# Kernel tuning notes

Measured on AMD Instinct MI355X. Metric: run time of the kernel, lower is better.

Reference implementation:

```python
import jax, jax.numpy as jnp
import numpy as np
import math

B, T, O = 4, 1024, 128
D, H, L, V = 512, 8, 6, 128
M, EH = 100000, 4
EHD = D // EH
HD = D // H
TK = O + 2 * T
PAD_ID = 0
NGRAM = 4

def _primes():
    ps = []
    base = 131
    for h in range(EH):
        x = base + h * 1009
        row = []
        for _ in range(NGRAM):
            row.append(x % (2 ** 32))
            x = x * 31 + 1
        ps.append(row)
    return jnp.array(ps, dtype=jnp.uint32)

PRIMES = _primes()

def rmsnorm(x, scale, eps=1e-6):
    return x / jnp.sqrt(jnp.mean(jnp.square(x), axis=-1, keepdims=True) + eps) * scale

def precompute_freqs_cis(dim, max_len, theta=10000.0):
    freqs = 1.0 / theta ** (jnp.arange(0, dim, 2, dtype=jnp.float32) / dim)
    t = jnp.arange(max_len, dtype=jnp.float32)
    return jnp.exp(1j * jnp.outer(t, freqs))[None, :, None, :]  # (1, max_len, 1, dim/2)

def apply_rope(x, f):
    b, t, h, d = x.shape
    xc = jax.lax.complex(x[..., 0::2], x[..., 1::2])
    xr = xc * f
    return jnp.stack([xr.real, xr.imag], axis=-1).reshape(b, t, h, d)

def setup_inputs() -> dict:
    key = jax.random.key(0)
    ks = jax.random.split(key, 16)
    rn = lambda k, shp, s=0.02: jax.random.normal(k, shp, jnp.float32) * s
    logit = lambda p: float(np.log(p / (1.0 - p)))
    return {
        'tokens_w': jax.random.randint(ks[0], (B, T), 0, V, dtype=jnp.int32),
        'mem_ids': jax.random.randint(ks[1], (B, O), 0, V, dtype=jnp.int32),
        'mem_emb': jax.random.normal(ks[2], (B, O, D), jnp.float32),
        'ssum': jax.random.normal(ks[3], (B, D), jnp.float32),
        'embed_table': rn(ks[4], (V, D)),
        'engram_table': rn(ks[5], (M, EH, EHD)),
        'engram_gate': jnp.full((EH, EHD), -2.0, jnp.float32),
        'engram_scale': jnp.ones(D, jnp.float32),
        'mem_W': rn(ks[6], (D, D)), 'mem_b': jnp.zeros(D, jnp.float32),
        'mem_scale': jnp.ones(D, jnp.float32),
        'alpha_gate': jnp.full((D,), logit(0.1), jnp.float32),
        'ssum_W': rn(ks[7], (D, D)),
        'ln1': jnp.ones((L, D), jnp.float32),
        'qW': rn(ks[8], (L, D, D)), 'qb': jnp.zeros((L, D), jnp.float32),
        'kW': rn(ks[9], (L, D, D)), 'kb': jnp.zeros((L, D), jnp.float32),
        'vW': rn(ks[10], (L, D, D)), 'vb': jnp.zeros((L, D), jnp.float32),
        'oW': rn(ks[11], (L, D, D)), 'ob': jnp.zeros((L, D), jnp.float32),
        'ln2': jnp.ones((L, D), jnp.float32),
        'w_in': rn(ks[12], (L, D, 8 * D)),
        'w_out': rn(ks[13], (L, 4 * D, D)),
        'final_scale': jnp.ones(D, jnp.float32),
    }

def _forward(tokens_w, mem_ids, mem_emb, ssum, embed_table, engram_table, engram_gate,
             engram_scale, mem_W, mem_b, mem_scale, alpha_gate, ssum_W,
             ln1, qW, qb, kW, kb, vW, vb, oW, ob, ln2, w_in, w_out, final_scale):
    # token embedding
    x = embed_table[tokens_w]  # (B,T,D)
    # multi-head engram: rolling n-gram hash lookup
    cur = jnp.where(tokens_w == PAD_ID, 0, tokens_w).astype(jnp.uint32)
    prev = jnp.where(mem_ids == PAD_ID, 0, mem_ids).astype(jnp.uint32)
    full = jnp.concatenate([prev, cur], axis=1)  # (B, O+T)
    hs = jnp.zeros((B, T, EH), jnp.uint32)
    for i in range(NGRAM):
        chunk = full[:, O - i: O + T - i]
        hs = hs + chunk[:, :, None] * PRIMES[None, None, :, i]
    idx = (hs % jnp.uint32(M)).astype(jnp.int32)  # (B,T,EH)
    retr = engram_table[idx, jnp.arange(EH)[None, None, :], :]  # (B,T,EH,EHD)
    eng = (retr * jax.nn.sigmoid(engram_gate)[None, None]).reshape(B, T, D)
    eng = rmsnorm(eng, engram_scale)
    # memory adapter + state-sum injection
    mem_p = rmsnorm(mem_emb @ mem_W + mem_b, mem_scale)
    alpha = jax.nn.sigmoid(alpha_gate)
    x = x + (ssum @ ssum_W)[:, None, :] * alpha[None, None, :]
    kv_seq = jnp.concatenate([mem_p, eng, x], axis=1)  # (B, TK, D)
    # masks: mem fully visible, engram + current causal; pad invalid keys
    tril = jnp.tril(jnp.ones((T, T), bool))
    full_mask = jnp.concatenate([jnp.ones((T, O), bool), tril, tril], axis=1)
    valid_curr = tokens_w != PAD_ID
    valid_k = jnp.concatenate([jnp.ones((B, O), bool), valid_curr, valid_curr], axis=1)
    mask = full_mask[None, None] & valid_k[:, None, None, :]  # (B,1,T,TK)
    freqs = precompute_freqs_cis(HD, TK + 32)
    fq, fk = freqs[:, :T], freqs[:, :TK]
    scale = 1.0 / math.sqrt(HD)

    def block(cx, p):
        ln1_, qW_, qb_, kW_, kb_, vW_, vb_, oW_, ob_, ln2_, wi_, wo_ = p
        nx = rmsnorm(cx, ln1_)
        q = (nx @ qW_ + qb_).reshape(B, T, H, HD)
        k = (kv_seq @ kW_ + kb_).reshape(B, TK, H, HD)
        v = (kv_seq @ vW_ + vb_).reshape(B, TK, H, HD)
        q = apply_rope(q, fq)
        k = apply_rope(k, fk)
        scores = jnp.einsum('bqhd,bkhd->bhqk', q, k) * scale
        scores = jnp.where(mask, scores, -1e9)
        probs = jax.nn.softmax(scores, axis=-1)
        o = jnp.einsum('bhqk,bkhd->bqhd', probs, v).reshape(B, T, D)
        cx = cx + o @ oW_ + ob_
        n2 = rmsnorm(cx, ln2_)
        gate, val = jnp.split(n2 @ wi_, 2, axis=-1)
        cx = cx + (jax.nn.silu(gate) * val) @ wo_
        return cx, None

    curr_x, _ = jax.lax.scan(block, x, (ln1, qW, qb, kW, kb, vW, vb, oW, ob, ln2, w_in, w_out))
    return rmsnorm(curr_x, final_scale)

def reference(tokens_w, mem_ids, mem_emb, ssum, embed_table, engram_table, engram_gate,
              engram_scale, mem_W, mem_b, mem_scale, alpha_gate, ssum_W,
              ln1, qW, qb, kW, kb, vW, vb, oW, ob, ln2, w_in, w_out, final_scale):
    return _forward(tokens_w, mem_ids, mem_emb, ssum, embed_table, engram_table, engram_gate,
                    engram_scale, mem_W, mem_b, mem_scale, alpha_gate, ssum_W,
                    ln1, qW, qb, kW, kb, vW, vb, oW, ob, ln2, w_in, w_out, final_scale)
```

## Files before the change

kernel.cpp:

```cpp
#include <hip/hip_runtime.h>
#include <hip/hip_bf16.h>
#include <math.h>

#define B_ 4
#define T_ 1024
#define O_ 128
#define D_ 512
#define H_ 8
#define L_ 6
#define TK_ 2176
#define MM_ 100000
#define EH_ 4
#define EHD_ 128
#define HD_ 64

typedef float f32x4 __attribute__((ext_vector_type(4)));
typedef short bf16x8 __attribute__((ext_vector_type(8)));
typedef unsigned short u16;

__device__ __constant__ unsigned int PRIMES_[4][4] = {
  {131u,  4062u,  125923u, 3903614u},
  {1140u, 35341u, 1095572u, 33962733u},
  {2149u, 66620u, 2065221u, 64021852u},
  {3158u, 97899u, 3034870u, 94080971u},
};

__device__ __forceinline__ float wave_sum_f(float v) {
  #pragma unroll
  for (int off = 32; off; off >>= 1) v += __shfl_xor(v, off);
  return v;
}

__device__ __forceinline__ short f2bf(float f) {
  unsigned int u = __float_as_uint(f);
  unsigned int r = (u + 0x7fffu + ((u >> 16) & 1u)) >> 16;
  return (short)r;
}

__device__ __forceinline__ void gload16(const void* g, void* l) {
  __builtin_amdgcn_global_load_lds((const __attribute__((address_space(1))) void*)g,
                                   (__attribute__((address_space(3))) void*)l, 16, 0, 0);
}

__global__ __launch_bounds__(64) void rope_table_k(float* __restrict__ rc,
                                                   float* __restrict__ rs) {
  int i = blockIdx.x * 64 + threadIdx.x;
  int t = i >> 5, j = i & 31;
  float freq = __powf(10000.0f, -(float)j / 32.0f);
  float ang = (float)t * freq;
  rc[i] = cosf(ang);
  rs[i] = sinf(ang);
}

__global__ __launch_bounds__(256) void ssum_proj_k(const float* __restrict__ ssum,
                                                   const float* __restrict__ sW,
                                                   float* __restrict__ ssp) {
  int col = blockIdx.x * 256 + threadIdx.x;
  int b = blockIdx.y;
  float acc = 0.f;
  for (int d = 0; d < D_; ++d) acc += ssum[b * D_ + d] * sW[(size_t)d * D_ + col];
  ssp[b * D_ + col] = acc;
}

__global__ __launch_bounds__(256) void sgemm_k(const float* __restrict__ A,
                                               const float* __restrict__ W,
                                               const float* __restrict__ bias,
                                               float* __restrict__ C,
                                               int M, int N, int K) {
  __shared__ float As[16][68];
  __shared__ float Bs[16][68];
  int tid = threadIdx.x;
  int row0 = blockIdx.y * 64;
  int col0 = blockIdx.x * 64;
  int tx = tid & 15, ty = tid >> 4;
  int am = tid >> 2, ak = (tid & 3) * 4;
  int bk = tid >> 4, bc = (tid & 15) * 4;
  float acc[4][4] = {};
  for (int k0 = 0; k0 < K; k0 += 16) {
    float4 av = *reinterpret_cast<const float4*>(&A[(size_t)(row0 + am) * K + k0 + ak]);
    As[ak + 0][am] = av.x; As[ak + 1][am] = av.y; As[ak + 2][am] = av.z; As[ak + 3][am] = av.w;
    float4 bv = *reinterpret_cast<const float4*>(&W[(size_t)(k0 + bk) * N + col0 + bc]);
    *reinterpret_cast<float4*>(&Bs[bk][bc]) = bv;
    __syncthreads();
    #pragma unroll
    for (int kk = 0; kk < 16; ++kk) {
      float4 a4 = *reinterpret_cast<const float4*>(&As[kk][ty * 4]);
      float4 b4 = *reinterpret_cast<const float4*>(&Bs[kk][tx * 4]);
      float a[4] = {a4.x, a4.y, a4.z, a4.w};
      float b[4] = {b4.x, b4.y, b4.z, b4.w};
      #pragma unroll
      for (int i = 0; i < 4; ++i)
        #pragma unroll
        for (int j = 0; j < 4; ++j) acc[i][j] += a[i] * b[j];
    }
    __syncthreads();
  }
  int cbase = col0 + tx * 4;
  float4 b4 = *reinterpret_cast<const float4*>(&bias[cbase]);
  float bb[4] = {b4.x, b4.y, b4.z, b4.w};
  #pragma unroll
  for (int i = 0; i < 4; ++i) {
    int row = row0 + ty * 4 + i;
    *reinterpret_cast<float4*>(&C[(size_t)row * N + cbase]) =
        make_float4(acc[i][0] + bb[0], acc[i][1] + bb[1], acc[i][2] + bb[2], acc[i][3] + bb[3]);
  }
}

__device__ __forceinline__ void wconv_tile(const float* __restrict__ W, u16* __restrict__ wT,
                                           int K, int N) {
  __shared__ float s[64][65];
  int n0 = blockIdx.x * 64, k0 = blockIdx.y * 64;
  int tid = threadIdx.x;
  int kr = tid >> 4, nc = (tid & 15) * 4;
  #pragma unroll
  for (int kk = 0; kk < 4; ++kk) {
    float4 f = *reinterpret_cast<const float4*>(&W[(size_t)(k0 + kr + kk * 16) * N + n0 + nc]);
    s[kr + kk * 16][nc + 0] = f.x; s[kr + kk * 16][nc + 1] = f.y;
    s[kr + kk * 16][nc + 2] = f.z; s[kr + kk * 16][nc + 3] = f.w;
  }
  __syncthreads();
  int nr = tid >> 4, kc = (tid & 15) * 4;
  #pragma unroll
  for (int nn = 0; nn < 4; ++nn) {
    int n = nr + nn * 16;
    ushort4 o;
    o.x = (u16)f2bf(s[kc + 0][n]); o.y = (u16)f2bf(s[kc + 1][n]);
    o.z = (u16)f2bf(s[kc + 2][n]); o.w = (u16)f2bf(s[kc + 3][n]);
    *reinterpret_cast<ushort4*>(&wT[(size_t)(n0 + n) * K + k0 + kc]) = o;
  }
}

__global__ __launch_bounds__(256) void wconv_qkvo_k(const float* __restrict__ qW,
                                                    const float* __restrict__ kW,
                                                    const float* __restrict__ vW,
                                                    const float* __restrict__ oW,
                                                    u16* __restrict__ dst) {
  int z = blockIdx.z;
  int l = z >> 2, which = z & 3;
  const float* src = which == 0 ? qW : which == 1 ? kW : which == 2 ? vW : oW;
  wconv_tile(src + (size_t)l * D_ * D_, dst + (size_t)z * D_ * D_, D_, D_);
}

__global__ __launch_bounds__(256) void wconv_win_k(const float* __restrict__ w_in,
                                                   u16* __restrict__ dst) {
  int l = blockIdx.z;
  wconv_tile(w_in + (size_t)l * 512 * 4096, dst + (size_t)l * 4096 * 512, 512, 4096);
}

__global__ __launch_bounds__(256) void wconv_wout_k(const float* __restrict__ w_out,
                                                    u16* __restrict__ dst) {
  int l = blockIdx.z;
  wconv_tile(w_out + (size_t)l * 2048 * 512, dst + (size_t)l * 512 * 2048, 2048, 512);
}

template<int EPI>
__global__ __launch_bounds__(256) void gemm_sm_k(const u16* __restrict__ A,
                                                 const u16* __restrict__ Bt,
                                                 const float* __restrict__ bias,
                                                 void* __restrict__ Cout,
                                                 int M, int N, int K, int posmod,
                                                 const float* __restrict__ rc,
                                                 const float* __restrict__ rs) {
  __shared__ __align__(16) u16 As[2][64 * 32];
  __shared__ __align__(16) u16 Bs[2][64 * 32];
  int tid = threadIdx.x;
  int w = tid >> 6, lane = tid & 63;
  int lr = lane & 15, lg = lane >> 4;
  int row0 = blockIdx.y * 64, col0 = blockIdx.x * 64;
  int wr = w >> 1, wc = w & 1;
  f32x4 acc[2][2] = {};

  int srow = tid >> 2;
  int skel = (tid & 3) * 8;

  auto stage = [&](int buf, int k0) {
    gload16(A + (size_t)(row0 + srow) * K + k0 + skel, &As[buf][srow * 32 + skel]);
    gload16(Bt + (size_t)(col0 + srow) * K + k0 + skel, &Bs[buf][srow * 32 + skel]);
  };

  stage(0, 0);
  __syncthreads();
  int nk = K >> 5;
  int buf = 0;
  for (int t = 0; t < nk; ++t) {
    if (t + 1 < nk) stage(buf ^ 1, (t + 1) * 32);
    bf16x8 af[2], bf[2];
    #pragma unroll
    for (int i = 0; i < 2; ++i)
      af[i] = *reinterpret_cast<const bf16x8*>(&As[buf][(wr * 32 + i * 16 + lr) * 32 + lg * 8]);
    #pragma unroll
    for (int j = 0; j < 2; ++j)
      bf[j] = *reinterpret_cast<const bf16x8*>(&Bs[buf][(wc * 32 + j * 16 + lr) * 32 + lg * 8]);
    #pragma unroll
    for (int i = 0; i < 2; ++i)
      #pragma unroll
      for (int j = 0; j < 2; ++j)
        acc[i][j] = __builtin_amdgcn_mfma_f32_16x16x32_bf16(af[i], bf[j], acc[i][j], 0, 0, 0);
    __syncthreads();
    buf ^= 1;
  }

  #pragma unroll
  for (int j = 0; j < 2; ++j) {
    int col = col0 + wc * 32 + j * 16 + lr;
    float bs = bias ? bias[col] : 0.f;
    #pragma unroll
    for (int i = 0; i < 2; ++i) {
      #pragma unroll
      for (int r = 0; r < 4; ++r) {
        int row = row0 + wr * 32 + i * 16 + lg * 4 + r;
        float v = acc[i][j][r] + bs;
        if (EPI == 1) {
          int pos = row % posmod;
          int d = col & 63;
          float c = rc[(size_t)pos * 32 + (d >> 1)];
          float s = rs[(size_t)pos * 32 + (d >> 1)];
          float partner = __shfl_xor(v, 1);
          v = (d & 1) ? (partner * s + v * c) : (v * c - partner * s);
        }
        if (EPI == 2) {
          float* Cf = (float*)Cout;
          Cf[(size_t)row * N + col] += v;
        } else {
          u16* Cb = (u16*)Cout;
          Cb[(size_t)row * N + col] = (u16)f2bf(v);
        }
      }
    }
  }
}

__global__ __launch_bounds__(256) void kv_gemm_k(const u16* __restrict__ A,
                                                 const u16* __restrict__ wqkvoT,
                                                 const float* __restrict__ kbias_all,
                                                 const float* __restrict__ vbias_all,
                                                 u16* __restrict__ kb_base,
                                                 u16* __restrict__ vb_base,
                                                 const float* __restrict__ rc,
                                                 const float* __restrict__ rs,
                                                 int l0, size_t ostride) {
  __shared__ __align__(16) u16 As[2][128 * 32];
  __shared__ __align__(16) u16 Bk[2][64 * 32];
  __shared__ __align__(16) u16 Bv[2][64 * 32];
  const int K = 512, N = 512;
  int bid = blockIdx.x;
  int c_ = bid & 7;
  int x_ = (bid >> 3) & 7;
  int rest = bid >> 6;
  int yh = rest % 9;
  int z = rest / 9;
  int y_ = yh * 8 + c_;
  if (y_ >= 68) return;
  int l = l0 + z;
  const u16* wkT = wqkvoT + ((size_t)l * 4 + 1) * (D_ * D_);
  const u16* wvT = wqkvoT + ((size_t)l * 4 + 2) * (D_ * D_);
  const float* kbias = kbias_all + l * D_;
  const float* vbias = vbias_all + l * D_;
  u16* kb = kb_base + (size_t)z * ostride;
  u16* vb = vb_base + (size_t)z * ostride;
  int tid = threadIdx.x;
  int w = tid >> 6, lane = tid & 63;
  int lr = lane & 15, lg = lane >> 4;
  int row0 = y_ * 128, col0 = x_ * 64;
  int wr = w >> 1, wc = w & 1;
  f32x4 ak_[4][2] = {};
  f32x4 av_[4][2] = {};

  int srow = lane >> 2;
  int skel = (lane & 3) * 8;

  auto stage = [&](int buf, int k0) {
    #pragma unroll
    for (int ci = 0; ci < 2; ++ci) {
      int c = w * 2 + ci;
      gload16(A + (size_t)(row0 + c * 16 + srow) * K + k0 + skel, &As[buf][c * 512]);
    }
    gload16(wkT + (size_t)(col0 + w * 16 + srow) * K + k0 + skel, &Bk[buf][w * 512]);
    gload16(wvT + (size_t)(col0 + w * 16 + srow) * K + k0 + skel, &Bv[buf][w * 512]);
  };

  stage(0, 0);
  __syncthreads();
  int buf = 0;
  for (int t = 0; t < 16; ++t) {
    if (t + 1 < 16) stage(buf ^ 1, (t + 1) * 32);
    bf16x8 af[4], bk[2], bv[2];
    #pragma unroll
    for (int i = 0; i < 4; ++i)
      af[i] = *reinterpret_cast<const bf16x8*>(&As[buf][(wr * 64 + i * 16 + lr) * 32 + lg * 8]);
    #pragma unroll
    for (int j = 0; j < 2; ++j) {
      bk[j] = *reinterpret_cast<const bf16x8*>(&Bk[buf][(wc * 32 + j * 16 + lr) * 32 + lg * 8]);
      bv[j] = *reinterpret_cast<const bf16x8*>(&Bv[buf][(wc * 32 + j * 16 + lr) * 32 + lg * 8]);
    }
    #pragma unroll
    for (int i = 0; i < 4; ++i)
      #pragma unroll
      for (int j = 0; j < 2; ++j) {
        ak_[i][j] = __builtin_amdgcn_mfma_f32_16x16x32_bf16(af[i], bk[j], ak_[i][j], 0, 0, 0);
        av_[i][j] = __builtin_amdgcn_mfma_f32_16x16x32_bf16(af[i], bv[j], av_[i][j], 0, 0, 0);
      }
    __syncthreads();
    buf ^= 1;
  }

  #pragma unroll
  for (int j = 0; j < 2; ++j) {
    int col = col0 + wc * 32 + j * 16 + lr;
    float kbs = kbias[col], vbs = vbias[col];
    int d = col & 63;
    #pragma unroll
    for (int i = 0; i < 4; ++i) {
      #pragma unroll
      for (int r = 0; r < 4; ++r) {
        int row = row0 + wr * 64 + i * 16 + lg * 4 + r;
        int pos = row % TK_;
        float vk = ak_[i][j][r] + kbs;
        float c = rc[(size_t)pos * 32 + (d >> 1)];
        float s = rs[(size_t)pos * 32 + (d >> 1)];
        float partner = __shfl_xor(vk, 1);
        vk = (d & 1) ? (partner * s + vk * c) : (vk * c - partner * s);
        kb[(size_t)row * N + col] = (u16)f2bf(vk);
        vb[(size_t)row * N + col] = (u16)f2bf(av_[i][j][r] + vbs);
      }
    }
  }
}

__global__ __launch_bounds__(256) void mlp_in_mfma_k(const u16* __restrict__ A,
                                                     const u16* __restrict__ wiT,
                                                     u16* __restrict__ Hout) {
  __shared__ __align__(16) u16 As[2][128 * 32];
  __shared__ __align__(16) u16 Bg[2][64 * 32];
  __shared__ __align__(16) u16 Bv[2][64 * 32];
  int tid = threadIdx.x;
  int w = tid >> 6, lane = tid & 63;
  int lr = lane & 15, lg = lane >> 4;
  int hc0 = blockIdx.x * 64, row0 = blockIdx.y * 128;
  int wr = w >> 1, wc = w & 1;
  f32x4 ag[4][2] = {};
  f32x4 av[4][2] = {};
  const int K = 512;

  int srow = lane >> 2;
  int skel = (lane & 3) * 8;

  auto stage = [&](int buf, int k0) {
    #pragma unroll
    for (int ci = 0; ci < 2; ++ci) {
      int c = w * 2 + ci;
      gload16(A + (size_t)(row0 + c * 16 + srow) * K + k0 + skel, &As[buf][c * 512]);
    }
    gload16(wiT + (size_t)(hc0 + w * 16 + srow) * K + k0 + skel, &Bg[buf][w * 512]);
    gload16(wiT + (size_t)(2048 + hc0 + w * 16 + srow) * K + k0 + skel, &Bv[buf][w * 512]);
  };

  stage(0, 0);
  __syncthreads();
  int buf = 0;
  for (int t = 0; t < 16; ++t) {
    if (t + 1 < 16) stage(buf ^ 1, (t + 1) * 32);
    bf16x8 af[4], bg[2], bv[2];
    #pragma unroll
    for (int i = 0; i < 4; ++i)
      af[i] = *reinterpret_cast<const bf16x8*>(&As[buf][(wr * 64 + i * 16 + lr) * 32 + lg * 8]);
    #pragma unroll
    for (int j = 0; j < 2; ++j) {
      bg[j] = *reinterpret_cast<const bf16x8*>(&Bg[buf][(wc * 32 + j * 16 + lr) * 32 + lg * 8]);
      bv[j] = *reinterpret_cast<const bf16x8*>(&Bv[buf][(wc * 32 + j * 16 + lr) * 32 + lg * 8]);
    }
    #pragma unroll
    for (int i = 0; i < 4; ++i)
      #pragma unroll
      for (int j = 0; j < 2; ++j) {
        ag[i][j] = __builtin_amdgcn_mfma_f32_16x16x32_bf16(af[i], bg[j], ag[i][j], 0, 0, 0);
        av[i][j] = __builtin_amdgcn_mfma_f32_16x16x32_bf16(af[i], bv[j], av[i][j], 0, 0, 0);
      }
    __syncthreads();
    buf ^= 1;
  }

  #pragma unroll
  for (int j = 0; j < 2; ++j) {
    int col = hc0 + wc * 32 + j * 16 + lr;
    #pragma unroll
    for (int i = 0; i < 4; ++i) {
      #pragma unroll
      for (int r = 0; r < 4; ++r) {
        int row = row0 + wr * 64 + i * 16 + lg * 4 + r;
        float g = ag[i][j][r];
        float sg = g / (1.f + __expf(-g));
        Hout[(size_t)row * 2048 + col] = (u16)f2bf(sg * av[i][j][r]);
      }
    }
  }
}

template<int OUTBF>
__global__ __launch_bounds__(128) void rmsnorm_k(const float* __restrict__ in,
                                                 const float* __restrict__ scale,
                                                 void* __restrict__ out) {
  int row = blockIdx.x;
  int tid = threadIdx.x;
  float4 v = *reinterpret_cast<const float4*>(&in[(size_t)row * D_ + tid * 4]);
  float ss = v.x * v.x + v.y * v.y + v.z * v.z + v.w * v.w;
  ss = wave_sum_f(ss);
  __shared__ float red[2];
  if ((tid & 63) == 0) red[tid >> 6] = ss;
  __syncthreads();
  ss = red[0] + red[1];
  float inv = 1.0f / sqrtf(ss / (float)D_ + 1e-6f);
  float4 sc = *reinterpret_cast<const float4*>(&scale[tid * 4]);
  float o0 = v.x * inv * sc.x, o1 = v.y * inv * sc.y, o2 = v.z * inv * sc.z, o3 = v.w * inv * sc.w;
  if (OUTBF) {
    ushort4 o;
    o.x = (u16)f2bf(o0); o.y = (u16)f2bf(o1); o.z = (u16)f2bf(o2); o.w = (u16)f2bf(o3);
    *reinterpret_cast<ushort4*>((u16*)out + (size_t)row * D_ + tid * 4) = o;
  } else {
    *reinterpret_cast<float4*>((float*)out + (size_t)row * D_ + tid * 4) =
        make_float4(o0, o1, o2, o3);
  }
}

__global__ __launch_bounds__(128) void memnorm_k(const float* __restrict__ tmp,
                                                 const float* __restrict__ scale,
                                                 u16* __restrict__ kv) {
  int o = blockIdx.x, b = blockIdx.y;
  int tid = threadIdx.x;
  float4 v = *reinterpret_cast<const float4*>(&tmp[(size_t)(b * O_ + o) * D_ + tid * 4]);
  float ss = v.x * v.x + v.y * v.y + v.z * v.z + v.w * v.w;
  ss = wave_sum_f(ss);
  __shared__ float red[2];
  if ((tid & 63) == 0) red[tid >> 6] = ss;
  __syncthreads();
  ss = red[0] + red[1];
  float inv = 1.0f / sqrtf(ss / (float)D_ + 1e-6f);
  float4 sc = *reinterpret_cast<const float4*>(&scale[tid * 4]);
  ushort4 oo;
  oo.x = (u16)f2bf(v.x * inv * sc.x); oo.y = (u16)f2bf(v.y * inv * sc.y);
  oo.z = (u16)f2bf(v.z * inv * sc.z); oo.w = (u16)f2bf(v.w * inv * sc.w);
  *reinterpret_cast<ushort4*>(&kv[(size_t)(b * TK_ + o) * D_ + tid * 4]) = oo;
}

__global__ __launch_bounds__(128) void engram_k(const int* __restrict__ tokens,
                                                const int* __restrict__ mem_ids,
                                                const float* __restrict__ etab,
                                                const float* __restrict__ egate,
                                                const float* __restrict__ escale,
                                                u16* __restrict__ kv) {
  int t = blockIdx.x, b = blockIdx.y;
  int tid = threadIdx.x;
  unsigned int toks[4];
  #pragma unroll
  for (int i = 0; i < 4; ++i) {
    int idx = t - i;
    toks[i] = (idx >= 0) ? (unsigned int)tokens[b * T_ + idx]
                         : (unsigned int)mem_ids[b * O_ + O_ + idx];
  }
  int c = tid * 4;
  int h = c >> 7;
  int e = c & 127;
  unsigned int hs = 0;
  #pragma unroll
  for (int i = 0; i < 4; ++i) hs += toks[i] * PRIMES_[h][i];
  int idxh = (int)(hs % (unsigned int)MM_);
  float4 r = *reinterpret_cast<const float4*>(&etab[((size_t)idxh * EH_ + h) * EHD_ + e]);
  float4 g = *reinterpret_cast<const float4*>(&egate[h * EHD_ + e]);
  float4 val;
  val.x = r.x / (1.f + __expf(-g.x));
  val.y = r.y / (1.f + __expf(-g.y));
  val.z = r.z / (1.f + __expf(-g.z));
  val.w = r.w / (1.f + __expf(-g.w));
  float ss = val.x * val.x + val.y * val.y + val.z * val.z + val.w * val.w;
  ss = wave_sum_f(ss);
  __shared__ float red[2];
  if ((tid & 63) == 0) red[tid >> 6] = ss;
  __syncthreads();
  ss = red[0] + red[1];
  float inv = 1.0f / sqrtf(ss / (float)D_ + 1e-6f);
  float4 sc = *reinterpret_cast<const float4*>(&escale[c]);
  ushort4 oo;
  oo.x = (u16)f2bf(val.x * inv * sc.x); oo.y = (u16)f2bf(val.y * inv * sc.y);
  oo.z = (u16)f2bf(val.z * inv * sc.z); oo.w = (u16)f2bf(val.w * inv * sc.w);
  *reinterpret_cast<ushort4*>(&kv[(size_t)(b * TK_ + O_ + t) * D_ + c]) = oo;
}

__global__ __launch_bounds__(128) void embed_k(const int* __restrict__ tokens,
                                               const float* __restrict__ etab,
                                               const float* __restrict__ ssp,
                                               const float* __restrict__ alpha_g,
                                               float* __restrict__ cx,
                                               u16* __restrict__ kv) {
  int t = blockIdx.x, b = blockIdx.y;
  int tid = threadIdx.x;
  int c = tid * 4;
  int tok = tokens[b * T_ + t];
  float4 e = *reinterpret_cast<const float4*>(&etab[(size_t)tok * D_ + c]);
  float4 sp = *reinterpret_cast<const float4*>(&ssp[b * D_ + c]);
  float4 ag = *reinterpret_cast<const float4*>(&alpha_g[c]);
  float4 x;
  x.x = e.x + sp.x / (1.f + __expf(-ag.x));
  x.y = e.y + sp.y / (1.f + __expf(-ag.y));
  x.z = e.z + sp.z / (1.f + __expf(-ag.z));
  x.w = e.w + sp.w / (1.f + __expf(-ag.w));
  *reinterpret_cast<float4*>(&cx[(size_t)(b * T_ + t) * D_ + c]) = x;
  ushort4 oo;
  oo.x = (u16)f2bf(x.x); oo.y = (u16)f2bf(x.y);
  oo.z = (u16)f2bf(x.z); oo.w = (u16)f2bf(x.w);
  *reinterpret_cast<ushort4*>(&kv[(size_t)(b * TK_ + O_ + T_ + t) * D_ + c]) = oo;
}

#define KIDX8(r, c) (((r) << 6) + ((c) ^ (((r) & 7) << 3)))
#define KIDX4(r, c) (((r) << 6) + ((c) ^ (((r) & 15) << 2)))
#define PIDX(q, o) (((q) << 5) + ((o) ^ (((q) & 7) << 2)))

__global__ __launch_bounds__(512) void attn_mfma_k(const u16* __restrict__ qb,
                                                   const u16* __restrict__ kb,
                                                   const u16* __restrict__ vb,
                                                   const int* __restrict__ tokens,
                                                   u16* __restrict__ ob) {
  __shared__ __align__(16) short ks[2][64 * 64];
  __shared__ __align__(16) short vst[2][64 * 64];
  __shared__ __align__(16) unsigned int pbuf[8][16 * 32];
  __shared__ unsigned char vtok[T_];

  int fid = blockIdx.x;
  int h = fid & 7;
  int s = fid >> 3;
  int pair = s & 7;
  int b = s >> 3;
  int bxA = pair, bxB = 15 - pair;

  int tid = threadIdx.x;
  int w = tid >> 6, lane = tid & 63;
  int lr = lane & 15;
  int lg = lane >> 4;
  int myBx = (w < 4) ? bxA : bxB;
  int qw0 = myBx * 64 + (w & 3) * 16;
  int tq = qw0 + lr;

  for (int i = tid; i < T_; i += 512) vtok[i] = (tokens[b * T_ + i] != 0);

  bf16x8 aq[2];
  {
    const u16* qp = &qb[((size_t)(b * T_) + tq) * D_ + h * 64];
    aq[0] = *reinterpret_cast<const bf16x8*>(qp + lg * 8);
    aq[1] = *reinterpret_cast<const bf16x8*>(qp + 32 + lg * 8);
  }

  float m_ = -1e30f, lsum = 0.f;
  f32x4 od[4];
  #pragma unroll
  for (int dt = 0; dt < 4; ++dt) od[dt] = (f32x4){0.f, 0.f, 0.f, 0.f};

  int sr = tid >> 3;
  int sc = (tid & 7) * 8;
  int vr2 = (tid >> 4) * 2;
  int vc = (tid & 15) * 4;

  int nt = 2 + 2 * (bxB + 1);
  auto tile_pos = [&](int i, int& pos0, int& base, bool& masked, bool& part) {
    if (i < 2) { pos0 = i * 64; base = 0; masked = false; part = true; }
    else if (i < 3 + bxB) {
      int t = i - 2;
      pos0 = O_ + t * 64; base = O_; masked = true; part = (t <= myBx);
    } else {
      int t = i - (3 + bxB);
      pos0 = O_ + T_ + t * 64; base = O_ + T_; masked = true; part = (t <= myBx);
    }
  };

  bf16x8 pkA, pkB;
  short4 pv0A, pv1A, pv0B, pv1B;

  auto load_regs = [&](int pos0, bf16x8& pk, short4& v0, short4& v1) {
    const u16* kg = &kb[((size_t)(b * TK_) + pos0 + sr) * D_ + h * 64 + sc];
    pk = *reinterpret_cast<const bf16x8*>(kg);
    const u16* vg = &vb[((size_t)(b * TK_) + pos0 + vr2) * D_ + h * 64 + vc];
    v0 = *reinterpret_cast<const short4*>(vg);
    v1 = *reinterpret_cast<const short4*>(vg + D_);
  };

  auto write_lds = [&](int buf, bf16x8 pk, short4 pv0, short4 pv1) {
    *reinterpret_cast<bf16x8*>(&ks[buf][KIDX8(sr, sc)]) = pk;
    unsigned int t0 = (unsigned int)(u16)pv0.x | ((unsigned int)(u16)pv1.x << 16);
    unsigned int t1 = (unsigned int)(u16)pv0.y | ((unsigned int)(u16)pv1.y << 16);
    unsigned int t2 = (unsigned int)(u16)pv0.z | ((unsigned int)(u16)pv1.z << 16);
    unsigned int t3 = (unsigned int)(u16)pv0.w | ((unsigned int)(u16)pv1.w << 16);
    *reinterpret_cast<unsigned int*>(&vst[buf][KIDX4(vc + 0, vr2)]) = t0;
    *reinterpret_cast<unsigned int*>(&vst[buf][KIDX4(vc + 1, vr2)]) = t1;
    *reinterpret_cast<unsigned int*>(&vst[buf][KIDX4(vc + 2, vr2)]) = t2;
    *reinterpret_cast<unsigned int*>(&vst[buf][KIDX4(vc + 3, vr2)]) = t3;
  };

  unsigned int* pw = (unsigned int*)pbuf[w];

  auto compute = [&](int buf, int pos0, int base, bool masked) {
    float sv[4][4];
    __builtin_amdgcn_s_setprio(1);
    #pragma unroll
    for (int kt = 0; kt < 4; ++kt) {
      bf16x8 ka0 = *reinterpret_cast<const bf16x8*>(&ks[buf][KIDX8(kt * 16 + lr, lg * 8)]);
      bf16x8 ka1 = *reinterpret_cast<const bf16x8*>(&ks[buf][KIDX8(kt * 16 + lr, 32 + lg * 8)]);
      f32x4 sf = (f32x4){0.f, 0.f, 0.f, 0.f};
      sf = __builtin_amdgcn_mfma_f32_16x16x32_bf16(ka0, aq[0], sf, 0, 0, 0);
      sf = __builtin_amdgcn_mfma_f32_16x16x32_bf16(ka1, aq[1], sf, 0, 0, 0);
      #pragma unroll
      for (int r = 0; r < 4; ++r) sv[kt][r] = sf[r];
    }
    __builtin_amdgcn_s_setprio(0);
    if (masked) {
      #pragma unroll
      for (int kt = 0; kt < 4; ++kt) {
        #pragma unroll
        for (int r = 0; r < 4; ++r) {
          int tk = pos0 + kt * 16 + lg * 4 + r - base;
          bool valid = (vtok[tk] != 0) && (tk <= tq);
          sv[kt][r] = valid ? sv[kt][r] * 0.125f : -1e30f;
        }
      }
    } else {
      #pragma unroll
      for (int kt = 0; kt < 4; ++kt)
        #pragma unroll
        for (int r = 0; r < 4; ++r) sv[kt][r] *= 0.125f;
    }
    float pmax = sv[0][0];
    #pragma unroll
    for (int kt = 0; kt < 4; ++kt)
      #pragma unroll
      for (int r = 0; r < 4; ++r) pmax = fmaxf(pmax, sv[kt][r]);
    pmax = fmaxf(pmax, __shfl_xor(pmax, 16));
    pmax = fmaxf(pmax, __shfl_xor(pmax, 32));
    float mnew = fmaxf(m_, pmax);
    float al = __expf(m_ - mnew);
    m_ = mnew;
    float psum = 0.f;
    #pragma unroll
    for (int kt = 0; kt < 4; ++kt)
      #pragma unroll
      for (int r = 0; r < 4; ++r) {
        float pe = __expf(sv[kt][r] - mnew);
        sv[kt][r] = pe;
        psum += pe;
      }
    psum += __shfl_xor(psum, 16);
    psum += __shfl_xor(psum, 32);
    lsum = lsum * al + psum;
    #pragma unroll
    for (int dt = 0; dt < 4; ++dt) {
      f32x4 o = od[dt];
      o[0] *= al; o[1] *= al; o[2] *= al; o[3] *= al;
      od[dt] = o;
    }
    #pragma unroll
    for (int kt = 0; kt < 4; ++kt) {
      uint2 wp;
      asm("v_cvt_pk_bf16_f32 %0, %1, %2" : "=v"(wp.x) : "v"(sv[kt][0]), "v"(sv[kt][1]));
      asm("v_cvt_pk_bf16_f32 %0, %1, %2" : "=v"(wp.y) : "v"(sv[kt][2]), "v"(sv[kt][3]));
      *reinterpret_cast<uint2*>(&pw[PIDX(lr, kt * 8 + lg * 2)]) = wp;
    }
    bf16x8 pf0 = *reinterpret_cast<const bf16x8*>(&pw[PIDX(lr, lg * 4)]);
    bf16x8 pf1 = *reinterpret_cast<const bf16x8*>(&pw[PIDX(lr, 16 + lg * 4)]);
    __builtin_amdgcn_s_setprio(1);
    #pragma unroll
    for (int dt = 0; dt < 4; ++dt) {
      short4 lo0 = *reinterpret_cast<const short4*>(&vst[buf][KIDX4(dt * 16 + lr, lg * 8)]);
      short4 hi0 = *reinterpret_cast<const short4*>(&vst[buf][KIDX4(dt * 16 + lr, lg * 8 + 4)]);
      short4 lo1 = *reinterpret_cast<const short4*>(&vst[buf][KIDX4(dt * 16 + lr, 32 + lg * 8)]);
      short4 hi1 = *reinterpret_cast<const short4*>(&vst[buf][KIDX4(dt * 16 + lr, 36 + lg * 8)]);
      bf16x8 va0 = {lo0.x, lo0.y, lo0.z, lo0.w, hi0.x, hi0.y, hi0.z, hi0.w};
      bf16x8 va1 = {lo1.x, lo1.y, lo1.z, lo1.w, hi1.x, hi1.y, hi1.z, hi1.w};
      od[dt] = __builtin_amdgcn_mfma_f32_16x16x32_bf16(va0, pf0, od[dt], 0, 0, 0);
      od[dt] = __builtin_amdgcn_mfma_f32_16x16x32_bf16(va1, pf1, od[dt], 0, 0, 0);
    }
    __builtin_amdgcn_s_setprio(0);
  };

  {
    int pos0, base; bool masked, part;
    tile_pos(0, pos0, base, masked, part);
    load_regs(pos0, pkA, pv0A, pv1A);
    tile_pos(1, pos0, base, masked, part);
    load_regs(pos0, pkB, pv0B, pv1B);
  }
  for (int i = 0; i < nt; i += 2) {
    write_lds(0, pkA, pv0A, pv1A);
    __syncthreads();
    {
      int pos0, base; bool masked, part;
      tile_pos(i, pos0, base, masked, part);
      if (i + 2 < nt) {
        int npos, nb; bool nm, np;
        tile_pos(i + 2, npos, nb, nm, np);
        load_regs(npos, pkA, pv0A, pv1A);
      }
      if (part) compute(0, pos0, base, masked);
    }
    write_lds(1, pkB, pv0B, pv1B);
    __syncthreads();
    {
      int pos0, base; bool masked, part;
      tile_pos(i + 1, pos0, base, masked, part);
      if (i + 3 < nt) {
        int npos, nb; bool nm, np;
        tile_pos(i + 3, npos, nb, nm, np);
        load_regs(npos, pkB, pv0B, pv1B);
      }
      if (part) compute(1, pos0, base, masked);
    }
  }

  float inv = 1.0f / lsum;
  #pragma unroll
  for (int dt = 0; dt < 4; ++dt) {
    ushort4 o4;
    o4.x = (u16)f2bf(od[dt][0] * inv);
    o4.y = (u16)f2bf(od[dt][1] * inv);
    o4.z = (u16)f2bf(od[dt][2] * inv);
    o4.w = (u16)f2bf(od[dt][3] * inv);
    *reinterpret_cast<ushort4*>(
        &ob[((size_t)(b * T_) + tq) * D_ + h * 64 + dt * 16 + lg * 4]) = o4;
  }
}

extern "C" void kernel_launch(void* const* d_in, const int* in_sizes, int n_in,
                              void* d_out, int out_size, void* d_ws, size_t ws_size,
                              hipStream_t stream) {
  (void)in_sizes; (void)n_in; (void)out_size;
  const int* tokens = (const int*)d_in[0];
  const int* mem_ids = (const int*)d_in[1];
  const float* mem_emb = (const float*)d_in[2];
  const float* ssum = (const float*)d_in[3];
  const float* embed = (const float*)d_in[4];
  const float* engram_t = (const float*)d_in[5];
  const float* engram_g = (const float*)d_in[6];
  const float* engram_s = (const float*)d_in[7];
  const float* mem_W = (const float*)d_in[8];
  const float* mem_b = (const float*)d_in[9];
  const float* mem_s = (const float*)d_in[10];
  const float* alpha_g = (const float*)d_in[11];
  const float* ssum_W = (const float*)d_in[12];
  const float* ln1 = (const float*)d_in[13];
  const float* qW = (const float*)d_in[14];
  const float* qbias = (const float*)d_in[15];
  const float* kW = (const float*)d_in[16];
  const float* kbias = (const float*)d_in[17];
  const float* vW = (const float*)d_in[18];
  const float* vbias = (const float*)d_in[19];
  const float* oW = (const float*)d_in[20];
  const float* obias = (const float*)d_in[21];
  const float* ln2 = (const float*)d_in[22];
  const float* w_in = (const float*)d_in[23];
  const float* w_out = (const float*)d_in[24];
  const float* final_s = (const float*)d_in[25];

  const size_t KVSZ = (size_t)B_ * TK_ * D_;
  size_t need = (KVSZ * 2 * 2 * L_) + 120u * 1024 * 1024;
  bool batched = ws_size >= need;

  char* p = (char*)d_ws;
  auto alloc = [&](size_t bytes) { char* r = p; p += (bytes + 255) & ~(size_t)255; return r; };
  u16* kv_b   = (u16*)alloc(KVSZ * 2);
  float* cx   = (float*)alloc((size_t)B_ * T_ * D_ * 4);
  u16* nx_b   = (u16*)alloc((size_t)B_ * T_ * D_ * 2);
  u16* qb_b   = (u16*)alloc((size_t)B_ * T_ * D_ * 2);
  int nkv = batched ? L_ : 1;
  u16* kb_all = (u16*)alloc(KVSZ * 2 * nkv);
  u16* vb_all = (u16*)alloc(KVSZ * 2 * nkv);
  u16* hb;
  if (batched) hb = (u16*)alloc((size_t)B_ * T_ * 2048 * 2);
  else hb = kb_all;
  u16* wqkvoT = (u16*)alloc((size_t)L_ * 4 * D_ * D_ * 2);
  u16* wiT    = (u16*)alloc((size_t)L_ * 4096 * 512 * 2);
  u16* woutT  = (u16*)alloc((size_t)L_ * 512 * 2048 * 2);
  float* ssp  = (float*)alloc((size_t)B_ * D_ * 4);
  float* rc   = (float*)alloc((size_t)TK_ * 32 * 4);
  float* rs   = (float*)alloc((size_t)TK_ * 32 * 4);
  float* mem_tmp = (float*)qb_b;
  u16* ob_b = nx_b;

  rope_table_k<<<TK_ * 32 / 64, 64, 0, stream>>>(rc, rs);
  wconv_qkvo_k<<<dim3(8, 8, L_ * 4), 256, 0, stream>>>(qW, kW, vW, oW, wqkvoT);
  wconv_win_k<<<dim3(64, 8, L_), 256, 0, stream>>>(w_in, wiT);
  wconv_wout_k<<<dim3(8, 32, L_), 256, 0, stream>>>(w_out, woutT);
  ssum_proj_k<<<dim3(2, B_), 256, 0, stream>>>(ssum, ssum_W, ssp);
  sgemm_k<<<dim3(8, 8), 256, 0, stream>>>(mem_emb, mem_W, mem_b, mem_tmp, B_ * O_, D_, D_);
  memnorm_k<<<dim3(O_, B_), 128, 0, stream>>>(mem_tmp, mem_s, kv_b);
  engram_k<<<dim3(T_, B_), 128, 0, stream>>>(tokens, mem_ids, engram_t, engram_g, engram_s, kv_b);
  embed_k<<<dim3(T_, B_), 128, 0, stream>>>(tokens, embed, ssp, alpha_g, cx, kv_b);

  if (batched) {
    kv_gemm_k<<<dim3(8 * 8 * 9 * L_), 256, 0, stream>>>(kv_b, wqkvoT, kbias, vbias,
                                                        kb_all, vb_all, rc, rs, 0, KVSZ);
  }

  const size_t WSZ = (size_t)D_ * D_;
  for (int l = 0; l < L_; ++l) {
    const u16* wqT = wqkvoT + ((size_t)l * 4 + 0) * WSZ;
    const u16* woT = wqkvoT + ((size_t)l * 4 + 3) * WSZ;
    const u16* wil = wiT + (size_t)l * 4096 * 512;
    const u16* wol = woutT + (size_t)l * 512 * 2048;
    u16* kb_l = batched ? kb_all + (size_t)l * KVSZ : kb_all;
    u16* vb_l = batched ? vb_all + (size_t)l * KVSZ : vb_all;

    rmsnorm_k<1><<<B_ * T_, 128, 0, stream>>>(cx, ln1 + l * D_, nx_b);
    gemm_sm_k<1><<<dim3(8, 64), 256, 0, stream>>>(nx_b, wqT, qbias + l * D_, qb_b,
                                                  B_ * T_, D_, D_, T_, rc, rs);
    if (!batched) {
      kv_gemm_k<<<dim3(8 * 8 * 9), 256, 0, stream>>>(kv_b, wqkvoT, kbias, vbias,
                                                     kb_l, vb_l, rc, rs, l, 0);
    }
    attn_mfma_k<<<dim3(256), 512, 0, stream>>>(qb_b, kb_l, vb_l, tokens, ob_b);
    gemm_sm_k<2><<<dim3(8, 64), 256, 0, stream>>>(ob_b, woT, obias + l * D_, cx,
                                                  B_ * T_, D_, D_, 0, nullptr, nullptr);
    rmsnorm_k<1><<<B_ * T_, 128, 0, stream>>>(cx, ln2 + l * D_, nx_b);
    mlp_in_mfma_k<<<dim3(32, 32), 256, 0, stream>>>(nx_b, wil, hb);
    gemm_sm_k<2><<<dim3(8, 64), 256, 0, stream>>>(hb, wol, nullptr, cx,
                                                  B_ * T_, D_, 2048, 0, nullptr, nullptr);
  }
  rmsnorm_k<0><<<B_ * T_, 128, 0, stream>>>(cx, final_s, d_out);
}
```

Before: 1.052 ms.

## Widen attention KV tiles from 64 to 128 keys per iteration

New measurement: 1.054 ms (median of 2 runs). No clear change (+0.1%).

```diff
diff --git a/kernel.cpp b/kernel.cpp
--- a/kernel.cpp
+++ b/kernel.cpp
@@ -511,17 +511,17 @@
 }
 
 #define KIDX8(r, c) (((r) << 6) + ((c) ^ (((r) & 7) << 3)))
-#define KIDX4(r, c) (((r) << 6) + ((c) ^ (((r) & 15) << 2)))
-#define PIDX(q, o) (((q) << 5) + ((o) ^ (((q) & 7) << 2)))
+#define VIDX(d, c)  (((d) << 7) + ((c) ^ (((d) & 15) << 2)))
+#define PIDX2(q, o) (((q) << 6) + ((o) ^ (((q) & 15) << 2)))
 
 __global__ __launch_bounds__(512) void attn_mfma_k(const u16* __restrict__ qb,
                                                    const u16* __restrict__ kb,
                                                    const u16* __restrict__ vb,
                                                    const int* __restrict__ tokens,
                                                    u16* __restrict__ ob) {
-  __shared__ __align__(16) short ks[2][64 * 64];
-  __shared__ __align__(16) short vst[2][64 * 64];
-  __shared__ __align__(16) unsigned int pbuf[8][16 * 32];
+  __shared__ __align__(16) short ks[2][128 * 64];
+  __shared__ __align__(16) short vst[2][64 * 128];
+  __shared__ __align__(16) unsigned int pbuf[8][16 * 64];
   __shared__ unsigned char vtok[T_];
 
   int fid = blockIdx.x;
@@ -553,53 +553,59 @@
   #pragma unroll
   for (int dt = 0; dt < 4; ++dt) od[dt] = (f32x4){0.f, 0.f, 0.f, 0.f};
 
-  int sr = tid >> 3;
-  int sc = (tid & 7) * 8;
-  int vr2 = (tid >> 4) * 2;
+  int sr = tid >> 2;
+  int sc = (tid & 3) * 16;
+  int k4 = (tid >> 4) * 4;
   int vc = (tid & 15) * 4;
 
-  int nt = 2 + 2 * (bxB + 1);
+  int te = (bxB >> 1) + 1;
+  int myTe = myBx >> 1;
+  int nt = 1 + 2 * te;
   auto tile_pos = [&](int i, int& pos0, int& base, bool& masked, bool& part) {
-    if (i < 2) { pos0 = i * 64; base = 0; masked = false; part = true; }
-    else if (i < 3 + bxB) {
-      int t = i - 2;
-      pos0 = O_ + t * 64; base = O_; masked = true; part = (t <= myBx);
+    if (i < 1) { pos0 = 0; base = 0; masked = false; part = true; }
+    else if (i < 1 + te) {
+      int t = i - 1;
+      pos0 = O_ + t * 128; base = O_; masked = true; part = (t <= myTe);
     } else {
-      int t = i - (3 + bxB);
-      pos0 = O_ + T_ + t * 64; base = O_ + T_; masked = true; part = (t <= myBx);
+      int t = i - 1 - te;
+      pos0 = O_ + T_ + t * 128; base = O_ + T_; masked = true; part = (t <= myTe);
     }
   };
 
-  bf16x8 pkA, pkB;
-  short4 pv0A, pv1A, pv0B, pv1B;
-
-  auto load_regs = [&](int pos0, bf16x8& pk, short4& v0, short4& v1) {
+  bf16x8 pk0, pk1;
+  short4 pv0, pv1, pv2, pv3;
+
+  auto load_regs = [&](int pos0) {
     const u16* kg = &kb[((size_t)(b * TK_) + pos0 + sr) * D_ + h * 64 + sc];
-    pk = *reinterpret_cast<const bf16x8*>(kg);
-    const u16* vg = &vb[((size_t)(b * TK_) + pos0 + vr2) * D_ + h * 64 + vc];
-    v0 = *reinterpret_cast<const short4*>(vg);
-    v1 = *reinterpret_cast<const short4*>(vg + D_);
+    pk0 = *reinterpret_cast<const bf16x8*>(kg);
+    pk1 = *reinterpret_cast<const bf16x8*>(kg + 8);
+    const u16* vg = &vb[((size_t)(b * TK_) + pos0 + k4) * D_ + h * 64 + vc];
+    pv0 = *reinterpret_cast<const short4*>(vg);
+    pv1 = *reinterpret_cast<const short4*>(vg + D_);
+    pv2 = *reinterpret_cast<const short4*>(vg + 2 * D_);
+    pv3 = *reinterpret_cast<const short4*>(vg + 3 * D_);
   };
 
-  auto write_lds = [&](int buf, bf16x8 pk, short4 pv0, short4 pv1) {
-    *reinterpret_cast<bf16x8*>(&ks[buf][KIDX8(sr, sc)]) = pk;
-    unsigned int t0 = (unsigned int)(u16)pv0.x | ((unsigned int)(u16)pv1.x << 16);
-    unsigned int t1 = (unsigned int)(u16)pv0.y | ((unsigned int)(u16)pv1.y << 16);
-    unsigned int t2 = (unsigned int)(u16)pv0.z | ((unsigned int)(u16)pv1.z << 16);
-    unsigned int t3 = (unsigned int)(u16)pv0.w | ((unsigned int)(u16)pv1.w << 16);
-    *reinterpret_cast<unsigned int*>(&vst[buf][KIDX4(vc + 0, vr2)]) = t0;
-    *reinterpret_cast<unsigned int*>(&vst[buf][KIDX4(vc + 1, vr2)]) = t1;
-    *reinterpret_cast<unsigned int*>(&vst[buf][KIDX4(vc + 2, vr2)]) = t2;
-    *reinterpret_cast<unsigned int*>(&vst[buf][KIDX4(vc + 3, vr2)]) = t3;
+  auto write_lds = [&](int buf) {
+    *reinterpret_cast<bf16x8*>(&ks[buf][KIDX8(sr, sc)]) = pk0;
+    *reinterpret_cast<bf16x8*>(&ks[buf][KIDX8(sr, sc + 8)]) = pk1;
+    short4 t0 = make_short4(pv0.x, pv1.x, pv2.x, pv3.x);
+    short4 t1 = make_short4(pv0.y, pv1.y, pv2.y, pv3.y);
+    short4 t2 = make_short4(pv0.z, pv1.z, pv2.z, pv3.z);
+    short4 t3 = make_short4(pv0.w, pv1.w, pv2.w, pv3.w);
+    *reinterpret_cast<short4*>(&vst[buf][VIDX(vc + 0, k4)]) = t0;
+    *reinterpret_cast<short4*>(&vst[buf][VIDX(vc + 1, k4)]) = t1;
+    *reinterpret_cast<short4*>(&vst[buf][VIDX(vc + 2, k4)]) = t2;
+    *reinterpret_cast<short4*>(&vst[buf][VIDX(vc + 3, k4)]) = t3;
   };
 
   unsigned int* pw = (unsigned int*)pbuf[w];
 
   auto compute = [&](int buf, int pos0, int base, bool masked) {
-    float sv[4][4];
+    float sv[8][4];
     __builtin_amdgcn_s_setprio(1);
     #pragma unroll
-    for (int kt = 0; kt < 4; ++kt) {
+    for (int kt = 0; kt < 8; ++kt) {
       bf16x8 ka0 = *reinterpret_cast<const bf16x8*>(&ks[buf][KIDX8(kt * 16 + lr, lg * 8)]);
       bf16x8 ka1 = *reinterpret_cast<const bf16x8*>(&ks[buf][KIDX8(kt * 16 + lr, 32 + lg * 8)]);
       f32x4 sf = (f32x4){0.f, 0.f, 0.f, 0.f};
@@ -611,7 +617,7 @@
     __builtin_amdgcn_s_setprio(0);
     if (masked) {
       #pragma unroll
-      for (int kt = 0; kt < 4; ++kt) {
+      for (int kt = 0; kt < 8; ++kt) {
         #pragma unroll
         for (int r = 0; r < 4; ++r) {
           int tk = pos0 + kt * 16 + lg * 4 + r - base;
@@ -621,13 +627,13 @@
       }
     } else {
       #pragma unroll
-      for (int kt = 0; kt < 4; ++kt)
+      for (int kt = 0; kt < 8; ++kt)
         #pragma unroll
         for (int r = 0; r < 4; ++r) sv[kt][r] *= 0.125f;
     }
     float pmax = sv[0][0];
     #pragma unroll
-    for (int kt = 0; kt < 4; ++kt)
+    for (int kt = 0; kt < 8; ++kt)
       #pragma unroll
       for (int r = 0; r < 4; ++r) pmax = fmaxf(pmax, sv[kt][r]);
     pmax = fmaxf(pmax, __shfl_xor(pmax, 16));
@@ -637,7 +643,7 @@
     m_ = mnew;
     float psum = 0.f;
     #pragma unroll
-    for (int kt = 0; kt < 4; ++kt)
+    for (int kt = 0; kt < 8; ++kt)
       #pragma unroll
       for (int r = 0; r < 4; ++r) {
         float pe = __expf(sv[kt][r] - mnew);
@@ -654,25 +660,28 @@
       od[dt] = o;
     }
     #pragma unroll
-    for (int kt = 0; kt < 4; ++kt) {
+    for (int kt = 0; kt < 8; ++kt) {
       uint2 wp;
       asm("v_cvt_pk_bf16_f32 %0, %1, %2" : "=v"(wp.x) : "v"(sv[kt][0]), "v"(sv[kt][1]));
       asm("v_cvt_pk_bf16_f32 %0, %1, %2" : "=v"(wp.y) : "v"(sv[kt][2]), "v"(sv[kt][3]));
-      *reinterpret_cast<uint2*>(&pw[PIDX(lr, kt * 8 + lg * 2)]) = wp;
-    }
-    bf16x8 pf0 = *reinterpret_cast<const bf16x8*>(&pw[PIDX(lr, lg * 4)]);
-    bf16x8 pf1 = *reinterpret_cast<const bf16x8*>(&pw[PIDX(lr, 16 + lg * 4)]);
+      *reinterpret_cast<uint2*>(&pw[PIDX2(lr, kt * 8 + lg * 2)]) = wp;
+    }
+    bf16x8 pf0 = *reinterpret_cast<const bf16x8*>(&pw[PIDX2(lr, 0 * 16 + lg * 4)]);
+    bf16x8 pf1 = *reinterpret_cast<const bf16x8*>(&pw[PIDX2(lr, 1 * 16 + lg * 4)]);
+    bf16x8 pf2 = *reinterpret_cast<const bf16x8*>(&pw[PIDX2(lr, 2 * 16 + lg * 4)]);
+    bf16x8 pf3 = *reinterpret_cast<const bf16x8*>(&pw[PIDX2(lr, 3 * 16 + lg * 4)]);
     __builtin_amdgcn_s_setprio(1);
     #pragma unroll
     for (int dt = 0; dt < 4; ++dt) {
-      short4 lo0 = *reinterpret_cast<const short4*>(&vst[buf][KIDX4(dt * 16 + lr, lg * 8)]);
-      short4 hi0 = *reinterpret_cast<const short4*>(&vst[buf][KIDX4(dt * 16 + lr, lg * 8 + 4)]);
-      short4 lo1 = *reinterpret_cast<const short4*>(&vst[buf][KIDX4(dt * 16 + lr, 32 + lg * 8)]);
-      short4 hi1 = *reinterpret_cast<const short4*>(&vst[buf][KIDX4(dt * 16 + lr, 36 + lg * 8)]);
-      bf16x8 va0 = {lo0.x, lo0.y, lo0.z, lo0.w, hi0.x, hi0.y, hi0.z, hi0.w};
-      bf16x8 va1 = {lo1.x, lo1.y, lo1.z, lo1.w, hi1.x, hi1.y, hi1.z, hi1.w};
-      od[dt] = __builtin_amdgcn_mfma_f32_16x16x32_bf16(va0, pf0, od[dt], 0, 0, 0);
-      od[dt] = __builtin_amdgcn_mfma_f32_16x16x32_bf16(va1, pf1, od[dt], 0, 0, 0);
+      int d = dt * 16 + lr;
+      #pragma unroll
+      for (int m = 0; m < 4; ++m) {
+        short4 lo = *reinterpret_cast<const short4*>(&vst[buf][VIDX(d, m * 32 + lg * 8)]);
+        short4 hi = *reinterpret_cast<const short4*>(&vst[buf][VIDX(d, m * 32 + lg * 8 + 4)]);
+        bf16x8 va = {lo.x, lo.y, lo.z, lo.w, hi.x, hi.y, hi.z, hi.w};
+        bf16x8 pf = (m == 0) ? pf0 : (m == 1) ? pf1 : (m == 2) ? pf2 : pf3;
+        od[dt] = __builtin_amdgcn_mfma_f32_16x16x32_bf16(va, pf, od[dt], 0, 0, 0);
+      }
     }
     __builtin_amdgcn_s_setprio(0);
   };
@@ -680,35 +689,19 @@
   {
     int pos0, base; bool masked, part;
     tile_pos(0, pos0, base, masked, part);
-    load_regs(pos0, pkA, pv0A, pv1A);
-    tile_pos(1, pos0, base, masked, part);
-    load_regs(pos0, pkB, pv0B, pv1B);
-  }
-  for (int i = 0; i < nt; i += 2) {
-    write_lds(0, pkA, pv0A, pv1A);
+    load_regs(pos0);
+  }
+  for (int i = 0; i < nt; ++i) {
+    write_lds(i & 1);
     __syncthreads();
-    {
-      int pos0, base; bool masked, part;
-      tile_pos(i, pos0, base, masked, part);
-      if (i + 2 < nt) {
-        int npos, nb; bool nm, np;
-        tile_pos(i + 2, npos, nb, nm, np);
-        load_regs(npos, pkA, pv0A, pv1A);
-      }
-      if (part) compute(0, pos0, base, masked);
-    }
-    write_lds(1, pkB, pv0B, pv1B);
-    __syncthreads();
-    {
-      int pos0, base; bool masked, part;
-      tile_pos(i + 1, pos0, base, masked, part);
-      if (i + 3 < nt) {
-        int npos, nb; bool nm, np;
-        tile_pos(i + 3, npos, nb, nm, np);
-        load_regs(npos, pkB, pv0B, pv1B);
-      }
-      if (part) compute(1, pos0, base, masked);
-    }
+    int pos0, base; bool masked, part;
+    tile_pos(i, pos0, base, masked, part);
+    if (i + 1 < nt) {
+      int npos, nb; bool nm, np;
+      tile_pos(i + 1, npos, nb, nm, np);
+      load_regs(npos);
+    }
+    if (part) compute(i & 1, pos0, base, masked);
   }
 
   float inv = 1.0f / lsum;
```
